# Optimization experiments

Measured on AMD Instinct MI355X. Metric: run time of the kernel, lower is better.

The kernel has to match this reference:

```python
import jax, jax.numpy as jnp
import numpy as np
import math

B, S, D, H, NF = 2, 2048, 1024, 16, 4
DH = D // H


def setup_inputs() -> dict:
    key = jax.random.key(0)
    ks = jax.random.split(key, 8)
    scale = 0.01 / math.sqrt(D)  # rough attenuated-kaiming scale for projections
    return {
        "x": jax.random.normal(ks[0], (B, S, D), dtype=jnp.float32),
        "weights": jax.random.uniform(ks[1], (1, NF), dtype=jnp.float32),
        "Wq": jax.random.normal(ks[2], (D, D), dtype=jnp.float32) * scale,
        "bq": jnp.zeros((D,), dtype=jnp.float32),
        "Wk": jax.random.normal(ks[3], (D, D), dtype=jnp.float32) * scale,
        "bk": jnp.zeros((D,), dtype=jnp.float32),
        "Wv": jax.random.normal(ks[4], (D, D), dtype=jnp.float32) * scale,
        "bv": jnp.zeros((D,), dtype=jnp.float32),
        "Wout": jax.random.normal(ks[5], (NF, D, D), dtype=jnp.float32) / math.sqrt(D),
        "bout": jnp.zeros((NF, D), dtype=jnp.float32),
    }


def reference(x, weights, Wq, bq, Wk, bk, Wv, bv, Wout, bout):
    # projections (torch Linear: x @ W.T + b)
    q = x @ Wq.T + bq  # [B,S,D]
    k = x @ Wk.T + bk
    v = x @ Wv.T + bv
    # split heads -> [B,H,S,DH]
    split = lambda t: t.reshape(B, S, H, DH).transpose(0, 2, 1, 3)
    q, k, v = split(q), split(k), split(v)
    # scores with causal additive mask of -10000 (as in get_attention_mask)
    scores = jnp.einsum("bhqd,bhkd->bhqk", q, k) / math.sqrt(DH)
    i = jnp.arange(S)
    causal = (i[None, :] <= i[:, None])  # [S,S] True where allowed
    mask = (1.0 - causal.astype(scores.dtype)) * -10000.0
    attn = jax.nn.softmax(scores + mask, axis=-1)
    # dropout is disabled (p=0.0)
    out = jnp.einsum("bhqk,bhkd->bhqd", attn, v)  # [B,H,S,DH]
    out = out.transpose(0, 2, 1, 3).reshape(B, S, D)
    # WeightedFunctions: per-function Linear(d,d) combined by weights[0]
    w0 = weights[0]  # [NF]
    Weff = jnp.einsum("f,fod->od", w0, Wout)  # [D,D]
    beff = w0 @ bout  # [D]
    return out @ Weff.T + beff
```

## Files before the change

### kernel.cpp

```cpp
#include <hip/hip_runtime.h>


typedef unsigned short u16;
typedef __bf16 bf16_t;
typedef bf16_t bf16x8 __attribute__((ext_vector_type(8)));
typedef bf16_t bf16x4 __attribute__((ext_vector_type(4)));
typedef float f32x4 __attribute__((ext_vector_type(4)));
typedef u16 u16x8 __attribute__((ext_vector_type(8)));
typedef u16 u16x4 __attribute__((ext_vector_type(4)));

#define DEV __device__ __forceinline__

DEV u16 f2bf(float f) {
  unsigned u = __float_as_uint(f);
  u += 0x7FFFu + ((u >> 16) & 1u);
  return (u16)(u >> 16);
}

DEV void async_ld16(const void* g, void* lds_wave_uniform) {
  __builtin_amdgcn_global_load_lds(
      (const __attribute__((address_space(1))) void*)g,
      (__attribute__((address_space(3))) void*)lds_wave_uniform, 16, 0, 0);
}

DEV int KF(int r) { return (r & 3) ^ ((r >> 2) & 1); }

__global__ __launch_bounds__(256) void prep_kernel(
    const float* __restrict__ x, const float* __restrict__ Wq,
    const float* __restrict__ Wk, const float* __restrict__ Wv,
    const float* __restrict__ w4, const float* __restrict__ Wout,
    const float* __restrict__ bout, u16* __restrict__ xbf,
    u16* __restrict__ wqkv, u16* __restrict__ Weff, float* __restrict__ beff) {
  constexpr int NX = 1048576;
  constexpr int NW = 262144;
  const int stride = gridDim.x * 256;
  for (int id = blockIdx.x * 256 + threadIdx.x; id < NX + 3 * NW + NW;
       id += stride) {
    if (id < NX) {
      const float4 v = ((const float4*)x)[id];
      u16x4 o;
      o[0] = f2bf(v.x); o[1] = f2bf(v.y); o[2] = f2bf(v.z); o[3] = f2bf(v.w);
      ((u16x4*)xbf)[id] = o;
    } else if (id < NX + 3 * NW) {
      const int wi = id - NX;
      const int which = wi >> 18, j = wi & (NW - 1);
      const float* src = which == 0 ? Wq : (which == 1 ? Wk : Wv);
      const float4 v = ((const float4*)src)[j];
      u16x4 o;
      o[0] = f2bf(v.x); o[1] = f2bf(v.y); o[2] = f2bf(v.z); o[3] = f2bf(v.w);
      ((u16x4*)wqkv)[wi] = o;
    } else {
      const int i = id - NX - 3 * NW;
      const float w0 = w4[0], w1 = w4[1], w2 = w4[2], w3 = w4[3];
      const float4* W = (const float4*)Wout;
      const float4 a = W[i], b1 = W[NW + i], b2 = W[2 * NW + i],
                   b3 = W[3 * NW + i];
      u16x4 o;
      o[0] = f2bf(w0 * a.x + w1 * b1.x + w2 * b2.x + w3 * b3.x);
      o[1] = f2bf(w0 * a.y + w1 * b1.y + w2 * b2.y + w3 * b3.y);
      o[2] = f2bf(w0 * a.z + w1 * b1.z + w2 * b2.z + w3 * b3.z);
      o[3] = f2bf(w0 * a.w + w1 * b1.w + w2 * b2.w + w3 * b3.w);
      ((u16x4*)Weff)[i] = o;
      if (i < 256) {
        const float4* B4 = (const float4*)bout;
        const float4 ba = B4[i], c1 = B4[256 + i], c2 = B4[512 + i],
                     c3 = B4[768 + i];
        float4 ob;
        ob.x = w0 * ba.x + w1 * c1.x + w2 * c2.x + w3 * c3.x;
        ob.y = w0 * ba.y + w1 * c1.y + w2 * c2.y + w3 * c3.y;
        ob.z = w0 * ba.z + w1 * c1.z + w2 * c2.z + w3 * c3.z;
        ob.w = w0 * ba.w + w1 * c1.w + w2 * c2.w + w3 * c3.w;
        ((float4*)beff)[i] = ob;
      }
    }
  }
}


#define GEMM_PIPELINE_LOOP(A_, B_, m0_, n0_, K_)                               \
  int rA[2], oA[2], dstc[2];                                                   \
  _Pragma("unroll") for (int j = 0; j < 2; ++j) {                              \
    const int c = (j * 4 + w) * 64 + lane;                                     \
    rA[j] = c >> 2;                                                            \
    oA[j] = ((c & 3) ^ KF(rA[j])) * 8;                                         \
    dstc[j] = (j * 4 + w) * 512;                                               \
  }                                                                            \
  auto stage = [&](int buf, int kt) {                                          \
    _Pragma("unroll") for (int j = 0; j < 2; ++j) {                            \
      async_ld16(A_ + (m0_ + rA[j]) * K_ + kt + oA[j],                         \
                 &LDS[buf * 4096 + dstc[j]]);                                  \
      async_ld16(B_ + (n0_ + rA[j]) * K_ + kt + oA[j],                         \
                 &LDS[12288 + buf * 4096 + dstc[j]]);                          \
    }                                                                          \
  };                                                                           \
  f32x4 acc[4][4] = {};                                                        \
  stage(0, 0);                                                                 \
  stage(1, 32);                                                                \
  const int nt = K_ / 32;                                                      \
  int cur = 0, stg = 2;                                                        \
  for (int t = 0; t < nt; ++t) {                                               \
    if (t == nt - 1)                                                           \
      asm volatile("s_waitcnt vmcnt(0)\ns_barrier" ::: "memory");              \
    else                                                                       \
      asm volatile("s_waitcnt vmcnt(4)\ns_barrier" ::: "memory");              \
    __builtin_amdgcn_sched_barrier(0);                                         \
    if (t + 2 < nt) stage(stg, (t + 2) * 32);                                  \
    bf16x8 af[4], bfr[4];                                                      \
    _Pragma("unroll") for (int i = 0; i < 4; ++i) {                            \
      const int ra = wr * 64 + i * 16 + l15;                                   \
      const int rb = wc * 64 + i * 16 + l15;                                   \
      af[i] = *(const bf16x8*)&LDS[cur * 4096 + ra * 32 + ((l4 ^ KF(ra)) * 8)];\
      bfr[i] = *(const bf16x8*)&LDS[12288 + cur * 4096 + rb * 32 +             \
                                    ((l4 ^ KF(rb)) * 8)];                      \
    }                                                                          \
    asm volatile("s_waitcnt lgkmcnt(0)" ::: "memory");                         \
    __builtin_amdgcn_sched_barrier(0);                                         \
    __builtin_amdgcn_s_setprio(1);                                             \
    _Pragma("unroll") for (int i = 0; i < 4; ++i)                              \
        _Pragma("unroll") for (int j = 0; j < 4; ++j)                          \
            acc[i][j] = __builtin_amdgcn_mfma_f32_16x16x32_bf16(               \
                af[i], bfr[j], acc[i][j], 0, 0, 0);                            \
    __builtin_amdgcn_s_setprio(0);                                             \
    cur = cur == 2 ? 0 : cur + 1;                                              \
    stg = stg == 2 ? 0 : stg + 1;                                              \
  }

__global__ __launch_bounds__(256) void gemm_bt_kernel(
    const u16* __restrict__ A, const u16* __restrict__ Bw,
    const float* __restrict__ bias, float* __restrict__ C, int M, int N, int K) {
  __shared__ u16 LDS[24576];
  const int tid = threadIdx.x;
  const int w = tid >> 6, lane = tid & 63;
  const int l15 = lane & 15, l4 = lane >> 4;
  const int wr = w >> 1, wc = w & 1;
  const long m0 = (long)blockIdx.y * 128, n0 = (long)blockIdx.x * 128;

  GEMM_PIPELINE_LOOP(A, Bw, m0, n0, K)

#pragma unroll
  for (int i = 0; i < 4; ++i) {
    const long row0 = m0 + wr * 64 + i * 16 + l4 * 4;
#pragma unroll
    for (int j = 0; j < 4; ++j) {
      const long col = n0 + wc * 64 + j * 16 + l15;
      const float bb = bias[col];
#pragma unroll
      for (int r = 0; r < 4; ++r)
        C[(row0 + r) * N + col] = acc[i][j][r] + bb;
    }
  }
}

__global__ __launch_bounds__(256) void gemm_qkv_kernel(
    const u16* __restrict__ A, const u16* __restrict__ Bw,
    const float* __restrict__ bq, const float* __restrict__ bk,
    const float* __restrict__ bv, u16* __restrict__ qo, u16* __restrict__ ko,
    u16* __restrict__ vt) {
  constexpr int K = 1024;
  __shared__ u16 LDS[24576];
  const int tid = threadIdx.x;
  const int w = tid >> 6, lane = tid & 63;
  const int l15 = lane & 15, l4 = lane >> 4;
  const int wr = w >> 1, wc = w & 1;
  const long m0 = (long)blockIdx.y * 128, n0 = (long)blockIdx.x * 128;
  const int seg = blockIdx.x >> 3;
  const float* bias = seg == 0 ? bq : (seg == 1 ? bk : bv);
  const float scale = seg == 0 ? 0.18033688011112042f : 1.0f;

  GEMM_PIPELINE_LOOP(A, Bw, m0, n0, K)

  __syncthreads();
  const long ccol0 = n0 - (long)seg * 1024;
  if (seg < 2) {
    u16* outp = seg == 0 ? qo : ko;
#pragma unroll
    for (int i = 0; i < 4; ++i) {
#pragma unroll
      for (int j = 0; j < 4; ++j) {
        const int colb = wc * 64 + j * 16 + l15;
        const float bb = bias[ccol0 + colb];
#pragma unroll
        for (int r = 0; r < 4; ++r) {
          const int row = wr * 64 + i * 16 + l4 * 4 + r;
          LDS[row * 128 + (colb ^ ((row & 15) << 3))] =
              f2bf((acc[i][j][r] + bb) * scale);
        }
      }
    }
    __syncthreads();
#pragma unroll
    for (int p = 0; p < 8; ++p) {
      const int cid = p * 256 + tid;
      const int row = cid >> 4, c = cid & 15;
      const u16x8 vch = *(const u16x8*)&LDS[row * 128 + ((c ^ (row & 15)) * 8)];
      *(u16x8*)&outp[(m0 + row) * 1024 + ccol0 + c * 8] = vch;
    }
  } else {
    const int b = (int)(m0 >> 11);
    const int s0 = (int)(m0 & 2047);
#pragma unroll
    for (int i = 0; i < 4; ++i) {
#pragma unroll
      for (int j = 0; j < 4; ++j) {
        const int colb = wc * 64 + j * 16 + l15;
        const float bb = bias[ccol0 + colb];
#pragma unroll
        for (int r = 0; r < 4; ++r) {
          const int row = wr * 64 + i * 16 + l4 * 4 + r;
          LDS[colb * 128 + (row ^ ((colb & 15) << 3))] = f2bf(acc[i][j][r] + bb);
        }
      }
    }
    __syncthreads();
#pragma unroll
    for (int p = 0; p < 8; ++p) {
      const int cid = p * 256 + tid;
      const int c = cid >> 4, r0 = (cid & 15) * 8;
      const u16x8 vch = *(const u16x8*)&LDS[c * 128 + (r0 ^ ((c & 15) << 3))];
      const int gcol = (int)ccol0 + c;
      const int h = gcol >> 6, d = gcol & 63;
      *(u16x8*)&vt[(size_t)((b * 16 + h) * 64 + d) * 2048 + s0 + r0] = vch;
    }
  }
}

__global__ __launch_bounds__(512, 6) void flash_kernel(
    const u16* __restrict__ Q, const u16* __restrict__ Kg,
    const u16* __restrict__ Vt, u16* __restrict__ O,
    u16* __restrict__ accP, float* __restrict__ mP, float* __restrict__ lP) {
  constexpr int S = 2048, D = 1024, DH = 64;
  __shared__ u16 Ks[2][4096];
  __shared__ u16 Vs[2][4096];
  __shared__ u16 Ps[8192];
  const int tid = threadIdx.x;
  const int w = tid >> 6, lane = tid & 63;
  const int l15 = lane & 15, l4 = lane >> 4;
  const int bh = blockIdx.y, b = bh >> 4, h = bh & 15;
  const int x = 23 - (int)blockIdx.x;
  int bi, kvlo, kvhi, seg;
  if (x < 8) {
    bi = x; seg = -1; kvlo = 0; kvhi = 2 * bi + 2;
  } else {
    const int idx = x - 8;
    bi = 8 + (idx >> 1); seg = idx & 1;
    kvlo = seg ? (bi + 1) : 0;
    kvhi = seg ? (2 * bi + 2) : (bi + 1);
  }
  const int qw = 128 * bi + w * 16;
  const int qtile = qw >> 6;

  const u16* Kbh = Kg + (size_t)b * S * D + h * DH;
  const u16* Vbh = Vt + (size_t)bh * DH * S;

  const int srow = tid >> 3;
  const int scol = ((tid & 7) ^ (srow & 7)) * 8;
  const int sw = l15 & 7;

  bf16x8 qf[2];
  {
    const u16* qp = Q + (size_t)(b * S + qw + l15) * D + h * DH + l4 * 8;
    qf[0] = *(const bf16x8*)qp;
    qf[1] = *(const bf16x8*)(qp + 32);
  }

  f32x4 acc_o[4] = {};
  float m_run = -3e38f, l_run = 0.f;

  async_ld16(Kbh + (size_t)(kvlo * 64 + srow) * D + scol, &Ks[0][w * 512]);
  async_ld16(Vbh + (size_t)srow * S + kvlo * 64 + scol, &Vs[0][w * 512]);
  __syncthreads();

  for (int it = kvlo; it < kvhi; ++it) {
    const int buf = (it - kvlo) & 1;
    if (it + 1 < kvhi) {
      async_ld16(Kbh + (size_t)((it + 1) * 64 + srow) * D + scol,
                 &Ks[buf ^ 1][w * 512]);
      async_ld16(Vbh + (size_t)srow * S + (it + 1) * 64 + scol,
                 &Vs[buf ^ 1][w * 512]);
    }
    if (it <= qtile) {
      f32x4 accs[4] = {};
      __builtin_amdgcn_s_setprio(1);
#pragma unroll
      for (int cb = 0; cb < 4; ++cb) {
        const int row = cb * 16 + l15;
        const bf16x8 kf0 = *(const bf16x8*)&Ks[buf][row * 64 + ((l4 ^ sw) * 8)];
        const bf16x8 kf1 =
            *(const bf16x8*)&Ks[buf][row * 64 + (((l4 + 4) ^ sw) * 8)];
        accs[cb] =
            __builtin_amdgcn_mfma_f32_16x16x32_bf16(kf0, qf[0], accs[cb], 0, 0, 0);
        accs[cb] =
            __builtin_amdgcn_mfma_f32_16x16x32_bf16(kf1, qf[1], accs[cb], 0, 0, 0);
      }
      __builtin_amdgcn_s_setprio(0);
      float mx = -3e38f;
      if (it == qtile) {
#pragma unroll
        for (int cb = 0; cb < 4; ++cb)
#pragma unroll
          for (int r = 0; r < 4; ++r) {
            float s_ = accs[cb][r];
            if (it * 64 + cb * 16 + l4 * 4 + r > qw + l15) s_ = -3e38f;
            accs[cb][r] = s_;
            mx = fmaxf(mx, s_);
          }
      } else {
#pragma unroll
        for (int cb = 0; cb < 4; ++cb)
#pragma unroll
          for (int r = 0; r < 4; ++r) mx = fmaxf(mx, accs[cb][r]);
      }
      if (!__all(mx - m_run <= 8.0f)) {
        mx = fmaxf(mx, __shfl_xor(mx, 16));
        mx = fmaxf(mx, __shfl_xor(mx, 32));
        const float mn = fmaxf(m_run, mx);
        const float corr = __builtin_amdgcn_exp2f(m_run - mn);
        m_run = mn;
        float cq[4];
#pragma unroll
        for (int r = 0; r < 4; ++r) cq[r] = __shfl(corr, l4 * 4 + r, 64);
#pragma unroll
        for (int db = 0; db < 4; ++db)
#pragma unroll
          for (int r = 0; r < 4; ++r) acc_o[db][r] *= cq[r];
        l_run *= corr;
      }
      float rs = 0.f;
#pragma unroll
      for (int cb = 0; cb < 4; ++cb)
#pragma unroll
        for (int r = 0; r < 4; ++r) {
          const float pv = __builtin_amdgcn_exp2f(accs[cb][r] - m_run);
          accs[cb][r] = pv;
          rs += pv;
        }
      l_run += rs;
#pragma unroll
      for (int cb = 0; cb < 4; ++cb) {
        bf16x4 pk = {(bf16_t)accs[cb][0], (bf16_t)accs[cb][1],
                     (bf16_t)accs[cb][2], (bf16_t)accs[cb][3]};
        const int chunk = (2 * cb + (l4 >> 1)) ^ sw;
        *(bf16x4*)&Ps[w * 1024 + l15 * 64 + chunk * 8 + (l4 & 1) * 4] = pk;
      }
      asm volatile("s_waitcnt lgkmcnt(0)" ::: "memory");
      bf16x8 pa[2];
#pragma unroll
      for (int mf = 0; mf < 2; ++mf) {
        const int chunk = (mf * 4 + l4) ^ sw;
        pa[mf] = *(const bf16x8*)&Ps[w * 1024 + l15 * 64 + chunk * 8];
      }
      __builtin_amdgcn_s_setprio(1);
#pragma unroll
      for (int db = 0; db < 4; ++db) {
        const int row = db * 16 + l15;
        const bf16x8 vf0 = *(const bf16x8*)&Vs[buf][row * 64 + ((l4 ^ sw) * 8)];
        const bf16x8 vf1 =
            *(const bf16x8*)&Vs[buf][row * 64 + (((l4 + 4) ^ sw) * 8)];
        acc_o[db] =
            __builtin_amdgcn_mfma_f32_16x16x32_bf16(pa[0], vf0, acc_o[db], 0, 0, 0);
        acc_o[db] =
            __builtin_amdgcn_mfma_f32_16x16x32_bf16(pa[1], vf1, acc_o[db], 0, 0, 0);
      }
      __builtin_amdgcn_s_setprio(0);
    }
    __syncthreads();
  }

  float l_tot = l_run;
  l_tot += __shfl_xor(l_tot, 16);
  l_tot += __shfl_xor(l_tot, 32);
  float lq[4];
  if (seg < 0) {
#pragma unroll
    for (int r = 0; r < 4; ++r) lq[r] = __shfl(l_tot, l4 * 4 + r, 64);
  }
#pragma unroll
  for (int db = 0; db < 4; ++db) {
#pragma unroll
    for (int r = 0; r < 4; ++r) {
      const int row = l4 * 4 + r;
      const int col = db * 16 + l15;
      const float v = seg < 0 ? acc_o[db][r] / lq[r] : acc_o[db][r];
      Ps[w * 1024 + row * 64 + (col ^ ((row & 7) << 3))] = f2bf(v);
    }
  }
  asm volatile("s_waitcnt lgkmcnt(0)" ::: "memory");
  if (seg < 0) {
#pragma unroll
    for (int j = 0; j < 2; ++j) {
      const int cid = j * 64 + lane;
      const int row = cid >> 3, c = cid & 7;
      const u16x8 vch =
          *(const u16x8*)&Ps[w * 1024 + row * 64 + ((c ^ (row & 7)) * 8)];
      *(u16x8*)&O[(size_t)(b * S + qw + row) * D + h * DH + c * 8] = vch;
    }
  } else {
    const size_t base = (size_t)seg * 32768 + (size_t)bh * 1024 + (qw - 1024);
#pragma unroll
    for (int j = 0; j < 2; ++j) {
      const int cid = j * 64 + lane;
      const int row = cid >> 3, c = cid & 7;
      const u16x8 vch =
          *(const u16x8*)&Ps[w * 1024 + row * 64 + ((c ^ (row & 7)) * 8)];
      *(u16x8*)&accP[(base + row) * 64 + c * 8] = vch;
    }
    if (l4 == 0) {
      mP[base + l15] = m_run;
      lP[base + l15] = l_tot;
    }
  }
}

__global__ __launch_bounds__(256) void combine_kernel(
    const u16* __restrict__ accP, const float* __restrict__ mP,
    const float* __restrict__ lP, u16* __restrict__ O) {
  const int id = blockIdx.x * 256 + threadIdx.x;
  const int row = id >> 3;
  const int c0 = (id & 7) * 8;
  const float m0 = mP[row], m1 = mP[32768 + row];
  const float l0 = lP[row], l1 = lP[32768 + row];
  const float M = fmaxf(m0, m1);
  const float e0 = __builtin_amdgcn_exp2f(m0 - M);
  const float e1 = __builtin_amdgcn_exp2f(m1 - M);
  const float inv = 1.f / (l0 * e0 + l1 * e1);
  const bf16_t* aP = (const bf16_t*)accP;
  const bf16x8 a0 = *(const bf16x8*)&aP[(size_t)row * 64 + c0];
  const bf16x8 a1 = *(const bf16x8*)&aP[(size_t)(32768 + row) * 64 + c0];
  const int bh = row >> 10, s = 1024 + (row & 1023);
  const int b = bh >> 4, h = bh & 15;
  bf16_t* out = (bf16_t*)O + (size_t)(b * 2048 + s) * 1024 + h * 64 + c0;
  bf16x8 o;
#pragma unroll
  for (int j = 0; j < 8; ++j)
    o[j] = (bf16_t)(((float)a0[j] * e0 + (float)a1[j] * e1) * inv);
  *(bf16x8*)out = o;
}

extern "C" void kernel_launch(void* const* d_in, const int* in_sizes, int n_in,
                              void* d_out, int out_size, void* d_ws, size_t ws_size,
                              hipStream_t stream) {
  (void)in_sizes; (void)n_in; (void)out_size;
  const float* x   = (const float*)d_in[0];
  const float* wts = (const float*)d_in[1];
  const float* Wq  = (const float*)d_in[2];
  const float* bq  = (const float*)d_in[3];
  const float* Wk  = (const float*)d_in[4];
  const float* bk  = (const float*)d_in[5];
  const float* Wv  = (const float*)d_in[6];
  const float* bv  = (const float*)d_in[7];
  const float* Wo  = (const float*)d_in[8];
  const float* bo  = (const float*)d_in[9];
  float* out = (float*)d_out;

  if (ws_size < 58724352) return;

  char* ws = (char*)d_ws;
  u16* xbf  = (u16*)(ws + 0);
  u16* qbf  = (u16*)(ws + 8388608);
  u16* kbf  = (u16*)(ws + 16777216);
  u16* vt   = (u16*)(ws + 33554432);
  u16* attn = (u16*)(ws + 41943040);
  u16* wqkv = (u16*)(ws + 50331648);
  u16* wob  = (u16*)(ws + 56623104);
  float* beff = (float*)(ws + 58720256);

  u16* accP = xbf;
  float* mP = (float*)(ws + 50331648);
  float* lP = mP + 65536;

  prep_kernel<<<2048, 256, 0, stream>>>(x, Wq, Wk, Wv, wts, Wo, bo,
                                        xbf, wqkv, wob, beff);
  gemm_qkv_kernel<<<dim3(24, 32), 256, 0, stream>>>(xbf, wqkv, bq, bk, bv,
                                                    qbf, kbf, vt);
  flash_kernel<<<dim3(24, 32), 512, 0, stream>>>(qbf, kbf, vt, attn,
                                                 accP, mP, lP);
  combine_kernel<<<1024, 256, 0, stream>>>(accP, mP, lP, attn);
  gemm_bt_kernel<<<dim3(8, 32), 256, 0, stream>>>(
      attn, wob, beff, out, 4096, 1024, 1024);
}
```

Baseline: 108.8 us.

## Restructure flash attention into balanced paired query tiles with triple-buffered KV

```diff
diff --git a/kernel.cpp b/kernel.cpp
--- a/kernel.cpp
+++ b/kernel.cpp
@@ -1,5 +1,4 @@
 #include <hip/hip_runtime.h>
-
 
 typedef unsigned short u16;
 typedef __bf16 bf16_t;
@@ -76,7 +75,6 @@
   }
 }
 
-
 #define GEMM_PIPELINE_LOOP(A_, B_, m0_, n0_, K_)                               \
   int rA[2], oA[2], dstc[2];                                                   \
   _Pragma("unroll") for (int j = 0; j < 2; ++j) {                              \
@@ -224,30 +222,25 @@
   }
 }
 
-__global__ __launch_bounds__(512, 6) void flash_kernel(
+__global__ __launch_bounds__(512) void flash_kernel(
     const u16* __restrict__ Q, const u16* __restrict__ Kg,
     const u16* __restrict__ Vt, u16* __restrict__ O,
     u16* __restrict__ accP, float* __restrict__ mP, float* __restrict__ lP) {
   constexpr int S = 2048, D = 1024, DH = 64;
-  __shared__ u16 Ks[2][4096];
-  __shared__ u16 Vs[2][4096];
-  __shared__ u16 Ps[8192];
+  __shared__ u16 Ks[3][4096];
+  __shared__ u16 Vs[3][4096];
+  __shared__ u16 Ps[8][2048];
   const int tid = threadIdx.x;
   const int w = tid >> 6, lane = tid & 63;
   const int l15 = lane & 15, l4 = lane >> 4;
   const int bh = blockIdx.y, b = bh >> 4, h = bh & 15;
-  const int x = 23 - (int)blockIdx.x;
-  int bi, kvlo, kvhi, seg;
-  if (x < 8) {
-    bi = x; seg = -1; kvlo = 0; kvhi = 2 * bi + 2;
-  } else {
-    const int idx = x - 8;
-    bi = 8 + (idx >> 1); seg = idx & 1;
-    kvlo = seg ? (bi + 1) : 0;
-    kvhi = seg ? (2 * bi + 2) : (bi + 1);
-  }
-  const int qw = 128 * bi + w * 16;
-  const int qtile = qw >> 6;
+  const int xb = blockIdx.x;
+  const int p = xb >> 1, seg = xb & 1;
+  const int p1len = seg ? 0 : 4 * p + 4;
+  const int kvoff = seg ? (14 - 4 * p) : 0;
+  const int TA = seg ? (7 - p) : p;
+  const int TB = 7 - p;
+  const int qbA_keep = TA * 256 + w * 32;
 
   const u16* Kbh = Kg + (size_t)b * S * D + h * DH;
   const u16* Vbh = Vt + (size_t)bh * DH * S;
@@ -256,30 +249,101 @@
   const int scol = ((tid & 7) ^ (srow & 7)) * 8;
   const int sw = l15 & 7;
 
-  bf16x8 qf[2];
-  {
-    const u16* qp = Q + (size_t)(b * S + qw + l15) * D + h * DH + l4 * 8;
-    qf[0] = *(const bf16x8*)qp;
-    qf[1] = *(const bf16x8*)(qp + 32);
-  }
-
-  f32x4 acc_o[4] = {};
-  float m_run = -3e38f, l_run = 0.f;
-
-  async_ld16(Kbh + (size_t)(kvlo * 64 + srow) * D + scol, &Ks[0][w * 512]);
-  async_ld16(Vbh + (size_t)srow * S + kvlo * 64 + scol, &Vs[0][w * 512]);
-  __syncthreads();
-
-  for (int it = kvlo; it < kvhi; ++it) {
-    const int buf = (it - kvlo) & 1;
-    if (it + 1 < kvhi) {
-      async_ld16(Kbh + (size_t)((it + 1) * 64 + srow) * D + scol,
-                 &Ks[buf ^ 1][w * 512]);
-      async_ld16(Vbh + (size_t)srow * S + (it + 1) * 64 + scol,
-                 &Vs[buf ^ 1][w * 512]);
-    }
-    if (it <= qtile) {
-      f32x4 accs[4] = {};
+  bf16x8 qf[2][2], qfB[2][2];
+#pragma unroll
+  for (int c = 0; c < 2; ++c) {
+    const u16* qp =
+        Q + (size_t)(b * S + qbA_keep + c * 16 + l15) * D + h * DH + l4 * 8;
+    qf[c][0] = *(const bf16x8*)qp;
+    qf[c][1] = *(const bf16x8*)(qp + 32);
+    qfB[c][0] = qf[c][0];
+    qfB[c][1] = qf[c][1];
+  }
+  if (!seg) {
+    const int qbB = TB * 256 + w * 32;
+#pragma unroll
+    for (int c = 0; c < 2; ++c) {
+      const u16* qp =
+          Q + (size_t)(b * S + qbB + c * 16 + l15) * D + h * DH + l4 * 8;
+      qfB[c][0] = *(const bf16x8*)qp;
+      qfB[c][1] = *(const bf16x8*)(qp + 32);
+    }
+  }
+
+  f32x4 acc_o[2][4] = {};
+  float m_run[2] = {-3e38f, -3e38f};
+  float l_run[2] = {0.f, 0.f};
+
+  int qb = qbA_keep;
+  int qt64w = TA * 4 + (w >> 1);
+
+  auto kv_of = [&](int j) { return (j < p1len) ? j : (j - p1len + kvoff); };
+  auto stage = [&](int kv, int buf) {
+    async_ld16(Kbh + (size_t)(kv * 64 + srow) * D + scol, &Ks[buf][w * 512]);
+    async_ld16(Vbh + (size_t)srow * S + kv * 64 + scol, &Vs[buf][w * 512]);
+  };
+
+  stage(kv_of(0), 0);
+  stage(kv_of(1), 1);
+
+  constexpr int NST = 18;
+  for (int j = 0; j < NST; ++j) {
+    if (j == NST - 1)
+      asm volatile("s_waitcnt vmcnt(0)\ns_barrier" ::: "memory");
+    else
+      asm volatile("s_waitcnt vmcnt(2)\ns_barrier" ::: "memory");
+    __builtin_amdgcn_sched_barrier(0);
+    if (j + 2 < NST) stage(kv_of(j + 2), (j + 2) % 3);
+
+    if (seg == 0 && j == p1len) {
+      float lt[2], lq[2][4];
+#pragma unroll
+      for (int c = 0; c < 2; ++c) {
+        float t = l_run[c];
+        t += __shfl_xor(t, 16);
+        t += __shfl_xor(t, 32);
+        lt[c] = t;
+#pragma unroll
+        for (int r = 0; r < 4; ++r) lq[c][r] = __shfl(lt[c], l4 * 4 + r, 64);
+      }
+#pragma unroll
+      for (int c = 0; c < 2; ++c)
+#pragma unroll
+        for (int db = 0; db < 4; ++db)
+#pragma unroll
+          for (int r = 0; r < 4; ++r) {
+            const int row = c * 16 + l4 * 4 + r;
+            const int col = db * 16 + l15;
+            Ps[w][row * 64 + (col ^ ((row & 7) << 3))] =
+                f2bf(acc_o[c][db][r] / lq[c][r]);
+          }
+      asm volatile("s_waitcnt lgkmcnt(0)" ::: "memory");
+#pragma unroll
+      for (int j4 = 0; j4 < 4; ++j4) {
+        const int cid = j4 * 64 + lane;
+        const int row = cid >> 3, c8 = cid & 7;
+        const u16x8 vch =
+            *(const u16x8*)&Ps[w][row * 64 + ((c8 ^ (row & 7)) * 8)];
+        *(u16x8*)&O[(size_t)(b * S + qbA_keep + row) * D + h * DH + c8 * 8] =
+            vch;
+      }
+#pragma unroll
+      for (int c = 0; c < 2; ++c) {
+        qf[c][0] = qfB[c][0];
+        qf[c][1] = qfB[c][1];
+        m_run[c] = -3e38f;
+        l_run[c] = 0.f;
+#pragma unroll
+        for (int db = 0; db < 4; ++db) acc_o[c][db] = f32x4{0.f, 0.f, 0.f, 0.f};
+      }
+      qb = TB * 256 + w * 32;
+      qt64w = TB * 4 + (w >> 1);
+    }
+
+    const int it = kv_of(j);
+    const int buf = j % 3;
+    if (it <= qt64w) {
+      f32x4 accs[2][4] = {};
       __builtin_amdgcn_s_setprio(1);
 #pragma unroll
       for (int cb = 0; cb < 4; ++cb) {
@@ -287,68 +351,88 @@
         const bf16x8 kf0 = *(const bf16x8*)&Ks[buf][row * 64 + ((l4 ^ sw) * 8)];
         const bf16x8 kf1 =
             *(const bf16x8*)&Ks[buf][row * 64 + (((l4 + 4) ^ sw) * 8)];
-        accs[cb] =
-            __builtin_amdgcn_mfma_f32_16x16x32_bf16(kf0, qf[0], accs[cb], 0, 0, 0);
-        accs[cb] =
-            __builtin_amdgcn_mfma_f32_16x16x32_bf16(kf1, qf[1], accs[cb], 0, 0, 0);
+#pragma unroll
+        for (int c = 0; c < 2; ++c) {
+          accs[c][cb] = __builtin_amdgcn_mfma_f32_16x16x32_bf16(
+              kf0, qf[c][0], accs[c][cb], 0, 0, 0);
+          accs[c][cb] = __builtin_amdgcn_mfma_f32_16x16x32_bf16(
+              kf1, qf[c][1], accs[c][cb], 0, 0, 0);
+        }
       }
       __builtin_amdgcn_s_setprio(0);
-      float mx = -3e38f;
-      if (it == qtile) {
+      float mx[2] = {-3e38f, -3e38f};
+      if (it == qt64w) {
+#pragma unroll
+        for (int c = 0; c < 2; ++c)
+#pragma unroll
+          for (int cb = 0; cb < 4; ++cb)
+#pragma unroll
+            for (int r = 0; r < 4; ++r) {
+              float s_ = accs[c][cb][r];
+              if (it * 64 + cb * 16 + l4 * 4 + r > qb + c * 16 + l15)
+                s_ = -3e38f;
+              accs[c][cb][r] = s_;
+              mx[c] = fmaxf(mx[c], s_);
+            }
+      } else {
+#pragma unroll
+        for (int c = 0; c < 2; ++c)
+#pragma unroll
+          for (int cb = 0; cb < 4; ++cb)
+#pragma unroll
+            for (int r = 0; r < 4; ++r) mx[c] = fmaxf(mx[c], accs[c][cb][r]);
+      }
+      if (!__all(fmaxf(mx[0] - m_run[0], mx[1] - m_run[1]) <= 8.0f)) {
+#pragma unroll
+        for (int c = 0; c < 2; ++c) {
+          float m = mx[c];
+          m = fmaxf(m, __shfl_xor(m, 16));
+          m = fmaxf(m, __shfl_xor(m, 32));
+          const float mn = fmaxf(m_run[c], m);
+          const float corr = __builtin_amdgcn_exp2f(m_run[c] - mn);
+          m_run[c] = mn;
+          float cq[4];
+#pragma unroll
+          for (int r = 0; r < 4; ++r) cq[r] = __shfl(corr, l4 * 4 + r, 64);
+#pragma unroll
+          for (int db = 0; db < 4; ++db)
+#pragma unroll
+            for (int r = 0; r < 4; ++r) acc_o[c][db][r] *= cq[r];
+          l_run[c] *= corr;
+        }
+      }
+#pragma unroll
+      for (int c = 0; c < 2; ++c) {
+        float rs = 0.f;
 #pragma unroll
         for (int cb = 0; cb < 4; ++cb)
 #pragma unroll
           for (int r = 0; r < 4; ++r) {
-            float s_ = accs[cb][r];
-            if (it * 64 + cb * 16 + l4 * 4 + r > qw + l15) s_ = -3e38f;
-            accs[cb][r] = s_;
-            mx = fmaxf(mx, s_);
+            const float pv = __builtin_amdgcn_exp2f(accs[c][cb][r] - m_run[c]);
+            accs[c][cb][r] = pv;
+            rs += pv;
           }
-      } else {
-#pragma unroll
-        for (int cb = 0; cb < 4; ++cb)
-#pragma unroll
-          for (int r = 0; r < 4; ++r) mx = fmaxf(mx, accs[cb][r]);
-      }
-      if (!__all(mx - m_run <= 8.0f)) {
-        mx = fmaxf(mx, __shfl_xor(mx, 16));
-        mx = fmaxf(mx, __shfl_xor(mx, 32));
-        const float mn = fmaxf(m_run, mx);
-        const float corr = __builtin_amdgcn_exp2f(m_run - mn);
-        m_run = mn;
-        float cq[4];
-#pragma unroll
-        for (int r = 0; r < 4; ++r) cq[r] = __shfl(corr, l4 * 4 + r, 64);
-#pragma unroll
-        for (int db = 0; db < 4; ++db)
-#pragma unroll
-          for (int r = 0; r < 4; ++r) acc_o[db][r] *= cq[r];
-        l_run *= corr;
-      }
-      float rs = 0.f;
-#pragma unroll
-      for (int cb = 0; cb < 4; ++cb)
-#pragma unroll
-        for (int r = 0; r < 4; ++r) {
-          const float pv = __builtin_amdgcn_exp2f(accs[cb][r] - m_run);
-          accs[cb][r] = pv;
-          rs += pv;
-        }
-      l_run += rs;
-#pragma unroll
-      for (int cb = 0; cb < 4; ++cb) {
-        bf16x4 pk = {(bf16_t)accs[cb][0], (bf16_t)accs[cb][1],
-                     (bf16_t)accs[cb][2], (bf16_t)accs[cb][3]};
-        const int chunk = (2 * cb + (l4 >> 1)) ^ sw;
-        *(bf16x4*)&Ps[w * 1024 + l15 * 64 + chunk * 8 + (l4 & 1) * 4] = pk;
-      }
+        l_run[c] += rs;
+      }
+#pragma unroll
+      for (int c = 0; c < 2; ++c)
+#pragma unroll
+        for (int cb = 0; cb < 4; ++cb) {
+          bf16x4 pk = {(bf16_t)accs[c][cb][0], (bf16_t)accs[c][cb][1],
+                       (bf16_t)accs[c][cb][2], (bf16_t)accs[c][cb][3]};
+          const int chunk = (2 * cb + (l4 >> 1)) ^ sw;
+          *(bf16x4*)&Ps[w][(c * 16 + l15) * 64 + chunk * 8 + (l4 & 1) * 4] = pk;
+        }
       asm volatile("s_waitcnt lgkmcnt(0)" ::: "memory");
-      bf16x8 pa[2];
-#pragma unroll
-      for (int mf = 0; mf < 2; ++mf) {
-        const int chunk = (mf * 4 + l4) ^ sw;
-        pa[mf] = *(const bf16x8*)&Ps[w * 1024 + l15 * 64 + chunk * 8];
-      }
+      bf16x8 pa[2][2];
+#pragma unroll
+      for (int c = 0; c < 2; ++c)
+#pragma unroll
+        for (int mf = 0; mf < 2; ++mf) {
+          const int chunk = (mf * 4 + l4) ^ sw;
+          pa[c][mf] =
+              *(const bf16x8*)&Ps[w][(c * 16 + l15) * 64 + chunk * 8];
+        }
       __builtin_amdgcn_s_setprio(1);
 #pragma unroll
       for (int db = 0; db < 4; ++db) {
@@ -356,57 +440,51 @@
         const bf16x8 vf0 = *(const bf16x8*)&Vs[buf][row * 64 + ((l4 ^ sw) * 8)];
         const bf16x8 vf1 =
             *(const bf16x8*)&Vs[buf][row * 64 + (((l4 + 4) ^ sw) * 8)];
-        acc_o[db] =
-            __builtin_amdgcn_mfma_f32_16x16x32_bf16(pa[0], vf0, acc_o[db], 0, 0, 0);
-        acc_o[db] =
-            __builtin_amdgcn_mfma_f32_16x16x32_bf16(pa[1], vf1, acc_o[db], 0, 0, 0);
+#pragma unroll
+        for (int c = 0; c < 2; ++c) {
+          acc_o[c][db] = __builtin_amdgcn_mfma_f32_16x16x32_bf16(
+              pa[c][0], vf0, acc_o[c][db], 0, 0, 0);
+          acc_o[c][db] = __builtin_amdgcn_mfma_f32_16x16x32_bf16(
+              pa[c][1], vf1, acc_o[c][db], 0, 0, 0);
+        }
       }
       __builtin_amdgcn_s_setprio(0);
     }
-    __syncthreads();
-  }
-
-  float l_tot = l_run;
-  l_tot += __shfl_xor(l_tot, 16);
-  l_tot += __shfl_xor(l_tot, 32);
-  float lq[4];
-  if (seg < 0) {
-#pragma unroll
-    for (int r = 0; r < 4; ++r) lq[r] = __shfl(l_tot, l4 * 4 + r, 64);
-  }
-#pragma unroll
-  for (int db = 0; db < 4; ++db) {
-#pragma unroll
-    for (int r = 0; r < 4; ++r) {
-      const int row = l4 * 4 + r;
-      const int col = db * 16 + l15;
-      const float v = seg < 0 ? acc_o[db][r] / lq[r] : acc_o[db][r];
-      Ps[w * 1024 + row * 64 + (col ^ ((row & 7) << 3))] = f2bf(v);
-    }
-  }
+  }
+
+  float lt[2];
+#pragma unroll
+  for (int c = 0; c < 2; ++c) {
+    float t = l_run[c];
+    t += __shfl_xor(t, 16);
+    t += __shfl_xor(t, 32);
+    lt[c] = t;
+  }
+#pragma unroll
+  for (int c = 0; c < 2; ++c)
+#pragma unroll
+    for (int db = 0; db < 4; ++db)
+#pragma unroll
+      for (int r = 0; r < 4; ++r) {
+        const int row = c * 16 + l4 * 4 + r;
+        const int col = db * 16 + l15;
+        Ps[w][row * 64 + (col ^ ((row & 7) << 3))] = f2bf(acc_o[c][db][r]);
+      }
   asm volatile("s_waitcnt lgkmcnt(0)" ::: "memory");
-  if (seg < 0) {
-#pragma unroll
-    for (int j = 0; j < 2; ++j) {
-      const int cid = j * 64 + lane;
-      const int row = cid >> 3, c = cid & 7;
-      const u16x8 vch =
-          *(const u16x8*)&Ps[w * 1024 + row * 64 + ((c ^ (row & 7)) * 8)];
-      *(u16x8*)&O[(size_t)(b * S + qw + row) * D + h * DH + c * 8] = vch;
-    }
-  } else {
-    const size_t base = (size_t)seg * 32768 + (size_t)bh * 1024 + (qw - 1024);
-#pragma unroll
-    for (int j = 0; j < 2; ++j) {
-      const int cid = j * 64 + lane;
-      const int row = cid >> 3, c = cid & 7;
-      const u16x8 vch =
-          *(const u16x8*)&Ps[w * 1024 + row * 64 + ((c ^ (row & 7)) * 8)];
-      *(u16x8*)&accP[(base + row) * 64 + c * 8] = vch;
-    }
-    if (l4 == 0) {
-      mP[base + l15] = m_run;
-      lP[base + l15] = l_tot;
+  const size_t base =
+      (size_t)seg * 32768 + (size_t)bh * 1024 + (TB * 256 + w * 32 - 1024);
+#pragma unroll
+  for (int j4 = 0; j4 < 4; ++j4) {
+    const int cid = j4 * 64 + lane;
+    const int row = cid >> 3, c8 = cid & 7;
+    const u16x8 vch = *(const u16x8*)&Ps[w][row * 64 + ((c8 ^ (row & 7)) * 8)];
+    *(u16x8*)&accP[(base + row) * 64 + c8 * 8] = vch;
+  }
+  if (l4 == 0) {
+#pragma unroll
+    for (int c = 0; c < 2; ++c) {
+      mP[base + c * 16 + l15] = m_run[c];
+      lP[base + c * 16 + l15] = lt[c];
     }
   }
 }
@@ -472,8 +550,8 @@
                                         xbf, wqkv, wob, beff);
   gemm_qkv_kernel<<<dim3(24, 32), 256, 0, stream>>>(xbf, wqkv, bq, bk, bv,
                                                     qbf, kbf, vt);
-  flash_kernel<<<dim3(24, 32), 512, 0, stream>>>(qbf, kbf, vt, attn,
-                                                 accP, mP, lP);
+  flash_kernel<<<dim3(8, 32), 512, 0, stream>>>(qbf, kbf, vt, attn,
+                                                accP, mP, lP);
   combine_kernel<<<1024, 256, 0, stream>>>(accP, mP, lP, attn);
   gemm_bt_kernel<<<dim3(8, 32), 256, 0, stream>>>(
       attn, wob, beff, out, 4096, 1024, 1024);
```

Result: no change. 109.3 us (+0.5%).
